# Optimization experiments

Hardware: AMD Instinct MI355X
Metric: run time of the kernel (lower is better)

Reference implementation:

```python
import jax, jax.numpy as jnp
import numpy as np

D_MODEL = 1024
D_HEAD = 64

def setup_inputs() -> dict:
    key = jax.random.key(0)
    ks = jax.random.split(key, 7)
    s = 1.0 / np.sqrt(D_MODEL)
    x = jax.random.normal(ks[0], (4, 4096, D_MODEL), dtype=jnp.float32)
    Wq = jax.random.uniform(ks[1], (D_MODEL, D_HEAD), jnp.float32, -s, s)
    bq = jax.random.uniform(ks[2], (D_HEAD,), jnp.float32, -s, s)
    Wk = jax.random.uniform(ks[3], (D_MODEL, D_HEAD), jnp.float32, -s, s)
    bk = jax.random.uniform(ks[4], (D_HEAD,), jnp.float32, -s, s)
    Wv = jax.random.uniform(ks[5], (D_MODEL, D_HEAD), jnp.float32, -s, s)
    bv = jax.random.uniform(ks[6], (D_HEAD,), jnp.float32, -s, s)
    return {"x": x, "Wq": Wq, "bq": bq, "Wk": Wk, "bk": bk, "Wv": Wv, "bv": bv}

def reference(x, Wq, bq, Wk, bk, Wv, bv):
    # x: [b, s, d_model] -> Q,K,V: [b, s, d_head]
    Q = jnp.einsum('bsd,dh->bsh', x, Wq) + bq
    K = jnp.einsum('bsd,dh->bsh', x, Wk) + bk
    V = jnp.einsum('bsd,dh->bsh', x, Wv) + bv
    scale = 1.0 / jnp.sqrt(jnp.asarray(D_HEAD, x.dtype))
    scores = jnp.einsum('bqh,bkh->bqk', Q, K) * scale  # [b, s, s]
    attn = jax.nn.softmax(scores, axis=-1)
    return jnp.einsum('bqk,bkh->bqh', attn, V)  # [b, s, d_head]
```

## Files before the change

kernel.cpp:

```cpp
#include <hip/hip_runtime.h>

typedef __bf16 bf16x8 __attribute__((ext_vector_type(8)));
typedef __bf16 bf16x4 __attribute__((ext_vector_type(4)));
typedef float f32x4 __attribute__((ext_vector_type(4)));
typedef unsigned short u16x8 __attribute__((ext_vector_type(8)));

union FragU { u16x8 u; bf16x8 b; };
union PackU { bf16x4 v; unsigned long long q; };

__device__ __forceinline__ unsigned short bfbits(float f) {
  __bf16 h = (__bf16)f;
  union { __bf16 h; unsigned short s; } cv; cv.h = h;
  return cv.s;
}

#define MFMA16(a, b, c) __builtin_amdgcn_mfma_f32_16x16x32_bf16((a), (b), (c), 0, 0, 0)

#define QSCALE 0.18033688011112042f

__global__ __launch_bounds__(256) void wt_kernel(
    const float* __restrict__ Wq, const float* __restrict__ Wk, const float* __restrict__ Wv,
    unsigned short* __restrict__ WF)
{
  const int m = blockIdx.x >> 5;
  const int c = blockIdx.x & 31;
  const float* W = (m == 0) ? Wq : ((m == 1) ? Wk : Wv);
  const int t = threadIdx.x >> 6;
  const int lane = threadIdx.x & 63;
  const int l15 = lane & 15;
  const int g = lane >> 4;
  unsigned short* dst = WF + ((((size_t)m * 32 + c) * 4 + t) * 64 + lane) * 8;
#pragma unroll
  for (int e = 0; e < 8; ++e)
    dst[e] = bfbits(W[(size_t)(32 * c + 8 * g + e) * 64 + (16 * t + l15)]);
}

__global__ __launch_bounds__(256, 1) void proj_kernel(
    const float* __restrict__ x, const unsigned short* __restrict__ WF,
    const float* __restrict__ bq, const float* __restrict__ bk, const float* __restrict__ bv,
    unsigned short* __restrict__ Qb, unsigned short* __restrict__ KF,
    unsigned short* __restrict__ VF)
{
  __shared__ __align__(16) unsigned short ldsW[4][6144];
  const int tid = threadIdx.x;
  const int lane = tid & 63;
  const int wid = tid >> 6;
  const int l15 = lane & 15;
  const int g = lane >> 4;
  const int row0 = blockIdx.x * 64 + wid * 16;

  f32x4 accQ[4], accK[4], accV[4];
  const f32x4 zero = {0.f, 0.f, 0.f, 0.f};
#pragma unroll
  for (int i = 0; i < 4; ++i) { accQ[i] = zero; accK[i] = zero; accV[i] = zero; }

  const float* xrow = x + (size_t)(row0 + l15) * 1024;
  f32x4 xx0[4], xx1[4];

#define WDMA(CC) { const int sl_ = (CC) & 3; \
    _Pragma("unroll") for (int m_ = 0; m_ < 3; ++m_) { \
      const unsigned short* gs_ = WF + ((((size_t)m_ * 32 + (CC)) * 4 + wid) * 64 + lane) * 8; \
      __builtin_amdgcn_global_load_lds( \
          (const __attribute__((address_space(1))) void*)gs_, \
          (__attribute__((address_space(3))) void*)&ldsW[sl_][(m_ * 4 + wid) * 512], \
          16, 0, 0); } }

#define PLDX(XB, C) { xx0[XB] = *(const f32x4*)(xrow + 32 * (C) + 8 * g); \
                      xx1[XB] = *(const f32x4*)(xrow + 32 * (C) + 8 * g + 4); }

#define SUBIT(CC, KK, WIMM, DOW, DOX) { \
    asm volatile("s_waitcnt vmcnt(" #WIMM ")" ::: "memory"); \
    __builtin_amdgcn_s_barrier(); \
    __builtin_amdgcn_sched_barrier(0); \
    if (DOW) WDMA((CC) + 3); \
    FragU xf; \
    _Pragma("unroll") for (int i_ = 0; i_ < 4; ++i_) { \
      xf.b[i_] = (__bf16)xx0[KK][i_]; xf.b[4 + i_] = (__bf16)xx1[KK][i_]; } \
    if (DOX) PLDX(KK, (CC) + 4); \
    { const int rs_ = (CC) & 3; \
      _Pragma("unroll") for (int t = 0; t < 4; ++t) { \
        const bf16x8 wq_ = *(const bf16x8*)&ldsW[rs_][(0 * 4 + t) * 512 + lane * 8]; \
        const bf16x8 wk_ = *(const bf16x8*)&ldsW[rs_][(1 * 4 + t) * 512 + lane * 8]; \
        const bf16x8 wv_ = *(const bf16x8*)&ldsW[rs_][(2 * 4 + t) * 512 + lane * 8]; \
        accQ[t] = MFMA16(xf.b, wq_, accQ[t]); \
        accK[t] = MFMA16(xf.b, wk_, accK[t]); \
        accV[t] = MFMA16(wv_, xf.b, accV[t]); } } }

  WDMA(0)
  __builtin_amdgcn_sched_barrier(0);
  WDMA(1) WDMA(2)
  PLDX(0, 0) PLDX(1, 1) PLDX(2, 2) PLDX(3, 3)

#pragma unroll 1
  for (int cb = 0; cb < 28; cb += 4) {
    SUBIT(cb + 0, 0, 10, 1, 1)
    SUBIT(cb + 1, 1, 10, 1, 1)
    SUBIT(cb + 2, 2, 10, 1, 1)
    SUBIT(cb + 3, 3, 10, 1, 1)
  }
  SUBIT(28, 0, 10, 1, 0)
  SUBIT(29, 1, 8, 0, 0)
  SUBIT(30, 2, 3, 0, 0)
  SUBIT(31, 3, 0, 0, 0)

  const int b = blockIdx.x >> 6;
  const int kt = blockIdx.x & 63;
  const int q0 = row0 & 4095;
  unsigned short* Qbase = Qb + (size_t)b * 4096 * 64;
#pragma unroll
  for (int t = 0; t < 4; ++t) {
    const int hh = 16 * t + l15;
    const float bqv = bq[hh];
#pragma unroll
    for (int r = 0; r < 4; ++r)
      Qbase[(size_t)(q0 + 4 * g + r) * 64 + hh] = bfbits((accQ[t][r] + bqv) * QSCALE);
  }
  unsigned short* KFb = KF + ((size_t)b * 64 + kt) * 4096;
  unsigned short* VFb = VF + ((size_t)b * 64 + kt) * 4096;
#pragma unroll
  for (int t = 0; t < 4; ++t) {
    const int hh = 16 * t + l15;
    const float bkv = bk[hh];
#pragma unroll
    for (int r = 0; r < 4; ++r) {
      KFb[(size_t)((wid * 2 + (t >> 1)) * 64 + (t & 1) * 32 + (l15 >> 3) * 16 + 4 * g + r) * 8 +
          (l15 & 7)] = bfbits(accK[t][r] + bkv);
      const int hv = 16 * t + 4 * g + r;
      VFb[(size_t)((t * 2 + (wid >> 1)) * 64 + (wid & 1) * 32 + (l15 >> 3) * 16 + 4 * g + r) * 8 +
          (l15 & 7)] = bfbits(accV[t][r] + bv[hv]);
    }
  }
}

__global__ __launch_bounds__(256, 2) void flash_kernel(
    const unsigned short* __restrict__ Qb, const unsigned short* __restrict__ KF,
    const unsigned short* __restrict__ VF, float* __restrict__ out)
{
  __shared__ __align__(16) unsigned char lds[36864];
  const int tid = threadIdx.x;
  const int lane = tid & 63;
  const int w = tid >> 6;
  const int l15 = lane & 15;
  const int g = lane >> 4;
  const int bid = blockIdx.x;
  const int xcd = bid & 7;
  const int b = xcd >> 1;
  const int qt = (bid >> 3) * 2 + (xcd & 1);
  const int q0 = qt * 32;

  const unsigned short* Qp = Qb + (size_t)b * 4096 * 64;
  const unsigned short* KFb = KF + (size_t)b * 262144;
  const unsigned short* VFb = VF + (size_t)b * 262144;

  const bf16x8 qfA0 = *(const bf16x8*)(Qp + (size_t)(q0 + l15) * 64 + 8 * g);
  const bf16x8 qfA1 = *(const bf16x8*)(Qp + (size_t)(q0 + l15) * 64 + 32 + 8 * g);
  const bf16x8 qfB0 = *(const bf16x8*)(Qp + (size_t)(q0 + 16 + l15) * 64 + 8 * g);
  const bf16x8 qfB1 = *(const bf16x8*)(Qp + (size_t)(q0 + 16 + l15) * 64 + 32 + 8 * g);

  f32x4 O_A[4], O_B[4];
  const f32x4 zero = {0.f, 0.f, 0.f, 0.f};
#pragma unroll
  for (int i = 0; i < 4; ++i) { O_A[i] = zero; O_B[i] = zero; }
  float mA = -INFINITY, lA = 0.f, mB = -INFINITY, lB = 0.f;
  unsigned short* PwA = (unsigned short*)lds + (w * 2 + 0) * 1152;
  unsigned short* PwB = (unsigned short*)lds + (w * 2 + 1) * 1152;

#define SM_HALF(S, mvar, lvar, OA, PW) { \
  float mt = fmaxf(fmaxf(S[0][0], S[0][1]), fmaxf(S[0][2], S[0][3])); \
  _Pragma("unroll") for (int t = 1; t < 4; ++t) \
    _Pragma("unroll") for (int r = 0; r < 4; ++r) mt = fmaxf(mt, S[t][r]); \
  mt = fmaxf(mt, __shfl_xor(mt, 16)); \
  mt = fmaxf(mt, __shfl_xor(mt, 32)); \
  if (!__all(mt <= mvar + 8.0f)) { \
    const float mnew = fmaxf(mvar, mt); \
    const float alpha = __builtin_amdgcn_exp2f(mvar - mnew); \
    mvar = mnew; lvar *= alpha; \
    _Pragma("unroll") for (int r = 0; r < 4; ++r) { \
      const float ar = __shfl(alpha, 4 * g + r); \
      OA[0][r] *= ar; OA[1][r] *= ar; OA[2][r] *= ar; OA[3][r] *= ar; } \
  } \
  float ps = 0.f; \
  _Pragma("unroll") for (int t = 0; t < 4; ++t) { \
    const float p0 = __builtin_amdgcn_exp2f(S[t][0] - mvar); \
    const float p1 = __builtin_amdgcn_exp2f(S[t][1] - mvar); \
    const float p2 = __builtin_amdgcn_exp2f(S[t][2] - mvar); \
    const float p3 = __builtin_amdgcn_exp2f(S[t][3] - mvar); \
    ps += (p0 + p1) + (p2 + p3); \
    PackU pk_; pk_.v[0] = (__bf16)p0; pk_.v[1] = (__bf16)p1; \
    pk_.v[2] = (__bf16)p2; pk_.v[3] = (__bf16)p3; \
    *(unsigned long long*)((PW) + l15 * 72 + 16 * t + 4 * g) = pk_.q; } \
  ps += __shfl_xor(ps, 16); \
  ps += __shfl_xor(ps, 32); \
  lvar += ps; }

#define FBODY(KT, KFC, KFN, DOLD) { \
    const unsigned short* Vt_ = VFb + (KT) * 4096; \
    bf16x8 vf[8]; \
    _Pragma("unroll") for (int j = 0; j < 8; ++j) \
      vf[j] = *(const bf16x8*)(Vt_ + (j * 64 + lane) * 8); \
    if (DOLD) { \
      const unsigned short* Ktn_ = KFb + ((KT) + 4) * 4096; \
      _Pragma("unroll") for (int j = 0; j < 8; ++j) \
        KFN[j] = *(const bf16x8*)(Ktn_ + (j * 64 + lane) * 8); \
    } \
    f32x4 S_A[4], S_B[4]; \
    _Pragma("unroll") for (int t = 0; t < 4; ++t) { \
      S_A[t] = zero; \
      S_A[t] = MFMA16(KFC[2 * t], qfA0, S_A[t]); \
      S_A[t] = MFMA16(KFC[2 * t + 1], qfA1, S_A[t]); \
      S_B[t] = zero; \
      S_B[t] = MFMA16(KFC[2 * t], qfB0, S_B[t]); \
      S_B[t] = MFMA16(KFC[2 * t + 1], qfB1, S_B[t]); \
    } \
    SM_HALF(S_A, mA, lA, O_A, PwA) \
    SM_HALF(S_B, mB, lB, O_B, PwB) \
    _Pragma("unroll") for (int s = 0; s < 2; ++s) { \
      const bf16x8 paA = *(const bf16x8*)(PwA + l15 * 72 + 32 * s + 8 * g); \
      const bf16x8 paB = *(const bf16x8*)(PwB + l15 * 72 + 32 * s + 8 * g); \
      _Pragma("unroll") for (int nt = 0; nt < 4; ++nt) { \
        O_A[nt] = MFMA16(paA, vf[2 * nt + s], O_A[nt]); \
        O_B[nt] = MFMA16(paB, vf[2 * nt + s], O_B[nt]); \
      } } }

  bf16x8 kfA[8], kfB[8];
  {
    const unsigned short* Kt0 = KFb + w * 4096;
#pragma unroll
    for (int j = 0; j < 8; ++j) kfA[j] = *(const bf16x8*)(Kt0 + (j * 64 + lane) * 8);
  }
#pragma unroll 1
  for (int kt = w; kt < 64; kt += 8) {
    FBODY(kt, kfA, kfB, 1)
    FBODY(kt + 4, kfB, kfA, (kt + 8 < 64))
  }

  __syncthreads();
  float* O_l = (float*)lds;
  float* mlp = (float*)(lds + 34816);
#pragma unroll
  for (int nt = 0; nt < 4; ++nt)
#pragma unroll
    for (int r = 0; r < 4; ++r) {
      O_l[((w * 2 + 0) * 16 + 4 * g + r) * 68 + 16 * nt + l15] = O_A[nt][r];
      O_l[((w * 2 + 1) * 16 + 4 * g + r) * 68 + 16 * nt + l15] = O_B[nt][r];
    }
  if (g == 0) {
    mlp[((w * 2 + 0) * 16 + l15) * 2] = mA; mlp[((w * 2 + 0) * 16 + l15) * 2 + 1] = lA;
    mlp[((w * 2 + 1) * 16 + l15) * 2] = mB; mlp[((w * 2 + 1) * 16 + l15) * 2 + 1] = lB;
  }
  __syncthreads();

  const int q = tid >> 3;
  const int h0 = (tid & 7) * 8;
  const int qh = q >> 4, qr = q & 15;
  float M = -INFINITY;
#pragma unroll
  for (int s = 0; s < 4; ++s) M = fmaxf(M, mlp[((s * 2 + qh) * 16 + qr) * 2]);
  float L = 0.f;
  f32x4 a0 = zero, a1 = zero;
#pragma unroll
  for (int s = 0; s < 4; ++s) {
    const int rowi = (s * 2 + qh) * 16 + qr;
    const float wgt = __builtin_amdgcn_exp2f(mlp[rowi * 2] - M);
    L += wgt * mlp[rowi * 2 + 1];
    const f32x4 o0 = *(const f32x4*)&O_l[rowi * 68 + h0];
    const f32x4 o1 = *(const f32x4*)&O_l[rowi * 68 + h0 + 4];
#pragma unroll
    for (int i = 0; i < 4; ++i) { a0[i] += wgt * o0[i]; a1[i] += wgt * o1[i]; }
  }
  const float inv = 1.0f / L;
  float* ob = out + ((size_t)b * 4096 + qt * 32 + q) * 64 + h0;
  f32x4 r0 = {a0[0] * inv, a0[1] * inv, a0[2] * inv, a0[3] * inv};
  f32x4 r1 = {a1[0] * inv, a1[1] * inv, a1[2] * inv, a1[3] * inv};
  *(f32x4*)ob = r0;
  *(f32x4*)(ob + 4) = r1;
}

extern "C" void kernel_launch(void* const* d_in, const int* in_sizes, int n_in,
                              void* d_out, int out_size, void* d_ws, size_t ws_size,
                              hipStream_t stream) {
  const float* x  = (const float*)d_in[0];
  const float* Wq = (const float*)d_in[1];
  const float* bq = (const float*)d_in[2];
  const float* Wk = (const float*)d_in[3];
  const float* bk = (const float*)d_in[4];
  const float* Wv = (const float*)d_in[5];
  const float* bv = (const float*)d_in[6];

  char* ws = (char*)d_ws;
  unsigned short* WF = (unsigned short*)ws;
  unsigned short* Qb = (unsigned short*)(ws + (512u << 10));
  unsigned short* KF = (unsigned short*)(ws + (512u << 10) + (2u << 20));
  unsigned short* VF = (unsigned short*)(ws + (512u << 10) + (4u << 20));
  float* out = (float*)d_out;

  hipLaunchKernelGGL(wt_kernel,    dim3(96),  dim3(256), 0, stream, Wq, Wk, Wv, WF);
  hipLaunchKernelGGL(proj_kernel,  dim3(256), dim3(256), 0, stream, x, WF, bq, bk, bv, Qb, KF, VF);
  hipLaunchKernelGGL(flash_kernel, dim3(512), dim3(256), 0, stream, Qb, KF, VF, out);
}
```

Measured before the change: 55.16 us.

## Process two query groups per 512-thread flash block sharing K/V streams

Each flash block now has 8 waves that cover 64 queries as two groups of 32. Within each group, 4 waves split the key tiles, and the grid is halved to 256 blocks. The two groups read the same K/V fragments close together in time, which should improve L1/L2 reuse. The final reduction runs in two serialized passes through the same LDS, one per group. The launch bound of 512 threads with 2 blocks per CU lowers the register budget per thread, which risks spills or lower MFMA throughput given the large register-resident K fragments and accumulators.

```diff
diff --git a/kernel.cpp b/kernel.cpp
--- a/kernel.cpp
+++ b/kernel.cpp
@@ -132,7 +132,7 @@
   }
 }
 
-__global__ __launch_bounds__(256, 2) void flash_kernel(
+__global__ __launch_bounds__(512, 2) void flash_kernel(
     const unsigned short* __restrict__ Qb, const unsigned short* __restrict__ KF,
     const unsigned short* __restrict__ VF, float* __restrict__ out)
 {
@@ -140,13 +140,15 @@
   const int tid = threadIdx.x;
   const int lane = tid & 63;
   const int w = tid >> 6;
+  const int qg = w >> 2;
+  const int ks = w & 3;
   const int l15 = lane & 15;
   const int g = lane >> 4;
   const int bid = blockIdx.x;
   const int xcd = bid & 7;
   const int b = xcd >> 1;
   const int qt = (bid >> 3) * 2 + (xcd & 1);
-  const int q0 = qt * 32;
+  const int q0 = qt * 64 + qg * 32;
 
   const unsigned short* Qp = Qb + (size_t)b * 4096 * 64;
   const unsigned short* KFb = KF + (size_t)b * 262144;
@@ -224,56 +226,58 @@
 
   bf16x8 kfA[8], kfB[8];
   {
-    const unsigned short* Kt0 = KFb + w * 4096;
+    const unsigned short* Kt0 = KFb + ks * 4096;
 #pragma unroll
     for (int j = 0; j < 8; ++j) kfA[j] = *(const bf16x8*)(Kt0 + (j * 64 + lane) * 8);
   }
 #pragma unroll 1
-  for (int kt = w; kt < 64; kt += 8) {
+  for (int kt = ks; kt < 64; kt += 8) {
     FBODY(kt, kfA, kfB, 1)
     FBODY(kt + 4, kfB, kfA, (kt + 8 < 64))
   }
 
-  __syncthreads();
   float* O_l = (float*)lds;
   float* mlp = (float*)(lds + 34816);
-#pragma unroll
-  for (int nt = 0; nt < 4; ++nt)
-#pragma unroll
-    for (int r = 0; r < 4; ++r) {
-      O_l[((w * 2 + 0) * 16 + 4 * g + r) * 68 + 16 * nt + l15] = O_A[nt][r];
-      O_l[((w * 2 + 1) * 16 + 4 * g + r) * 68 + 16 * nt + l15] = O_B[nt][r];
+  const int q = tid >> 4;
+  const int h0 = (tid & 15) * 4;
+  const int qh = q >> 4, qr = q & 15;
+
+#pragma unroll 1
+  for (int pass = 0; pass < 2; ++pass) {
+    __syncthreads();
+    if (qg == pass) {
+#pragma unroll
+      for (int nt = 0; nt < 4; ++nt)
+#pragma unroll
+        for (int r = 0; r < 4; ++r) {
+          O_l[((ks * 2 + 0) * 16 + 4 * g + r) * 68 + 16 * nt + l15] = O_A[nt][r];
+          O_l[((ks * 2 + 1) * 16 + 4 * g + r) * 68 + 16 * nt + l15] = O_B[nt][r];
+        }
+      if (g == 0) {
+        mlp[((ks * 2 + 0) * 16 + l15) * 2] = mA; mlp[((ks * 2 + 0) * 16 + l15) * 2 + 1] = lA;
+        mlp[((ks * 2 + 1) * 16 + l15) * 2] = mB; mlp[((ks * 2 + 1) * 16 + l15) * 2 + 1] = lB;
+      }
     }
-  if (g == 0) {
-    mlp[((w * 2 + 0) * 16 + l15) * 2] = mA; mlp[((w * 2 + 0) * 16 + l15) * 2 + 1] = lA;
-    mlp[((w * 2 + 1) * 16 + l15) * 2] = mB; mlp[((w * 2 + 1) * 16 + l15) * 2 + 1] = lB;
-  }
-  __syncthreads();
-
-  const int q = tid >> 3;
-  const int h0 = (tid & 7) * 8;
-  const int qh = q >> 4, qr = q & 15;
-  float M = -INFINITY;
-#pragma unroll
-  for (int s = 0; s < 4; ++s) M = fmaxf(M, mlp[((s * 2 + qh) * 16 + qr) * 2]);
-  float L = 0.f;
-  f32x4 a0 = zero, a1 = zero;
-#pragma unroll
-  for (int s = 0; s < 4; ++s) {
-    const int rowi = (s * 2 + qh) * 16 + qr;
-    const float wgt = __builtin_amdgcn_exp2f(mlp[rowi * 2] - M);
-    L += wgt * mlp[rowi * 2 + 1];
-    const f32x4 o0 = *(const f32x4*)&O_l[rowi * 68 + h0];
-    const f32x4 o1 = *(const f32x4*)&O_l[rowi * 68 + h0 + 4];
-#pragma unroll
-    for (int i = 0; i < 4; ++i) { a0[i] += wgt * o0[i]; a1[i] += wgt * o1[i]; }
-  }
-  const float inv = 1.0f / L;
-  float* ob = out + ((size_t)b * 4096 + qt * 32 + q) * 64 + h0;
-  f32x4 r0 = {a0[0] * inv, a0[1] * inv, a0[2] * inv, a0[3] * inv};
-  f32x4 r1 = {a1[0] * inv, a1[1] * inv, a1[2] * inv, a1[3] * inv};
-  *(f32x4*)ob = r0;
-  *(f32x4*)(ob + 4) = r1;
+    __syncthreads();
+    float M = -INFINITY;
+#pragma unroll
+    for (int s = 0; s < 4; ++s) M = fmaxf(M, mlp[((s * 2 + qh) * 16 + qr) * 2]);
+    float L = 0.f;
+    f32x4 a0 = zero;
+#pragma unroll
+    for (int s = 0; s < 4; ++s) {
+      const int rowi = (s * 2 + qh) * 16 + qr;
+      const float wgt = __builtin_amdgcn_exp2f(mlp[rowi * 2] - M);
+      L += wgt * mlp[rowi * 2 + 1];
+      const f32x4 o0 = *(const f32x4*)&O_l[rowi * 68 + h0];
+#pragma unroll
+      for (int i = 0; i < 4; ++i) a0[i] += wgt * o0[i];
+    }
+    const float inv = 1.0f / L;
+    float* ob = out + ((size_t)b * 4096 + qt * 64 + pass * 32 + q) * 64 + h0;
+    f32x4 r0 = {a0[0] * inv, a0[1] * inv, a0[2] * inv, a0[3] * inv};
+    *(f32x4*)ob = r0;
+  }
 }
 
 extern "C" void kernel_launch(void* const* d_in, const int* in_sizes, int n_in,
@@ -296,5 +300,5 @@
 
   hipLaunchKernelGGL(wt_kernel,    dim3(96),  dim3(256), 0, stream, Wq, Wk, Wv, WF);
   hipLaunchKernelGGL(proj_kernel,  dim3(256), dim3(256), 0, stream, x, WF, bq, bk, bv, Qb, KF, VF);
-  hipLaunchKernelGGL(flash_kernel, dim3(512), dim3(256), 0, stream, Qb, KF, VF, out);
-}
+  hipLaunchKernelGGL(flash_kernel, dim3(256), dim3(512), 0, stream, Qb, KF, VF, out);
+}
```

Measured after the change: 55.34 us, median of 2. About the same (+0.3%).
